# Kernel optimization log

Measured on AMD Instinct MI355X. Metric: run time of the kernel, lower is better.

The kernel has to match this reference:

```python
import math
import jax, jax.numpy as jnp
import numpy as np

LMAX = 2


def _cg_complex(j1, m1, j2, m2, j3, m3):
    # Standard (Racah) Clebsch-Gordan coefficient <j1 m1 j2 m2 | j3 m3> for integer l.
    if m1 + m2 != m3 or j3 < abs(j1 - j2) or j3 > j1 + j2:
        return 0.0
    f = math.factorial
    pre = math.sqrt((2 * j3 + 1) * f(j3 + j1 - j2) * f(j3 - j1 + j2) * f(j1 + j2 - j3) / f(j1 + j2 + j3 + 1))
    pre *= math.sqrt(f(j3 + m3) * f(j3 - m3) * f(j1 - m1) * f(j1 + m1) * f(j2 - m2) * f(j2 + m2))
    kmin = max(0, j2 - j3 - m1, j1 + m2 - j3)
    kmax = min(j1 + j2 - j3, j1 - m1, j2 + m2)
    s = 0.0
    for k in range(kmin, kmax + 1):
        s += (-1.0) ** k / (f(k) * f(j1 + j2 - j3 - k) * f(j1 - m1 - k) * f(j2 + m2 - k) * f(j3 - j2 + m1 + k) * f(j3 - j1 - m2 + k))
    return pre * s


def _u_matrix(l):
    # Unitary map from complex SH (Condon-Shortley) to real SH, rows = real mu, cols = complex m.
    U = np.zeros((2 * l + 1, 2 * l + 1), dtype=np.complex128)
    U[l, l] = 1.0
    isq2 = 1.0 / math.sqrt(2.0)
    for m in range(1, l + 1):
        U[l + m, l - m] = isq2
        U[l + m, l + m] = ((-1.0) ** m) * isq2
        U[l - m, l - m] = 1j * isq2
        U[l - m, l + m] = -1j * ((-1.0) ** m) * isq2
    return U


def _real_clebsch_gordan(lmax):
    # Dense real-SH CG tensor over combined s=(l,m) indices, shape [S,S,S], S=(lmax+1)^2.
    S = (lmax + 1) ** 2
    cg = np.zeros((S, S, S))
    for l1 in range(lmax + 1):
        for l2 in range(lmax + 1):
            for l3 in range(abs(l1 - l2), min(lmax, l1 + l2) + 1):
                blk = np.zeros((2 * l1 + 1, 2 * l2 + 1, 2 * l3 + 1))
                for i1, m1 in enumerate(range(-l1, l1 + 1)):
                    for i2, m2 in enumerate(range(-l2, l2 + 1)):
                        for i3, m3 in enumerate(range(-l3, l3 + 1)):
                            blk[i1, i2, i3] = _cg_complex(l1, m1, l2, m2, l3, m3)
                U1, U2, U3 = _u_matrix(l1), _u_matrix(l2), _u_matrix(l3)
                r = np.einsum('am,bn,co,mno->abc', U1, U2, U3.conj(), blk.astype(np.complex128))
                r = r.real if (l1 + l2 + l3) % 2 == 0 else r.imag  # parity-dependent real part
                cg[l1 * l1:(l1 + 1) ** 2, l2 * l2:(l2 + 1) ** 2, l3 * l3:(l3 + 1) ** 2] = r
    return cg


def _sparse_cg(lmax):
    cg = _real_clebsch_gordan(lmax)
    i1, i2, i3 = np.nonzero(np.abs(cg) > 1e-10)
    vals = cg[i1, i2, i3].astype(np.float32)
    widx = np.floor(np.sqrt(i3.astype(np.float64))).astype(np.int32)  # l of output combined index
    return vals, i1.astype(np.int32), i2.astype(np.int32), i3.astype(np.int32), widx


def _spherical_harmonics_l2(d):
    # Real SH up to l=2, 'component' normalization (|x|=1 assumed). Order: (l,m) = (0,0),(1,-1),(1,0),(1,1),(2,-2..2).
    x, y, z = d[..., 0], d[..., 1], d[..., 2]
    s3, s5, s15 = math.sqrt(3.0), math.sqrt(5.0), math.sqrt(15.0)
    return jnp.stack([
        jnp.ones_like(x),
        s3 * y, s3 * z, s3 * x,
        s15 * x * y, s15 * y * z, 0.5 * s5 * (3.0 * z * z - 1.0), s15 * x * z, 0.5 * s15 * (x * x - y * y),
    ], axis=-1)


def setup_inputs():
    N_ATOMS, N_EDGES, N_BASIS, N_RADIAL = 1200, 12000, 128, 20
    S = (LMAX + 1) ** 2
    key = jax.random.key(0)
    ks = jax.random.split(key, 8)
    vals, i1, i2, i3, widx = _sparse_cg(LMAX)
    return {
        'x': jax.random.normal(ks[0], (N_ATOMS, S, N_BASIS), jnp.float32),
        'radial_ij': jax.random.uniform(ks[1], (N_EDGES, N_RADIAL), jnp.float32),
        'dir_ij': jax.random.normal(ks[2], (N_EDGES, 3), jnp.float32),
        'cutoff_ij': jax.random.uniform(ks[3], (N_EDGES, 1), jnp.float32),
        'W_filter': jax.random.normal(ks[6], (N_RADIAL, N_BASIS * (LMAX + 1)), jnp.float32) / math.sqrt(N_RADIAL),
        'b_filter': jnp.zeros((N_BASIS * (LMAX + 1),), jnp.float32),
        'cg_vals': jnp.asarray(vals),
        'idx_i': jax.random.randint(ks[4], (N_EDGES,), 0, N_ATOMS),
        'idx_j': jax.random.randint(ks[5], (N_EDGES,), 0, N_ATOMS),
        'cg_idx_in1': jnp.asarray(i1),
        'cg_idx_in2': jnp.asarray(i2),
        'cg_idx_out': jnp.asarray(i3),
        'w_idx': jnp.asarray(widx),
    }


def reference(x, radial_ij, dir_ij, cutoff_ij, W_filter, b_filter, cg_vals,
              idx_i, idx_j, cg_idx_in1, cg_idx_in2, cg_idx_out, w_idx):
    n_atoms, S, F = x.shape
    E = dir_ij.shape[0]
    d = dir_ij / jnp.linalg.norm(dir_ij, axis=-1, keepdims=True)
    Y = _spherical_harmonics_l2(d)                        # [E, S]
    Wij = (radial_ij @ W_filter + b_filter) * cutoff_ij   # [E, (lmax+1)*F]
    Wij = Wij.reshape(E, LMAX + 1, F)                     # per-l radial filter
    xj = x[idx_j]                                         # [E, S, F] neighbor features
    # Sparse CG tensor-product contraction over combined (l,m) indices.
    v = (Y[:, cg_idx_in2, None] * cg_vals[None, :, None]
         * Wij[:, w_idx, :] * xj[:, cg_idx_in1, :])       # [E, n_cg, F]
    yij = jnp.zeros((E, S, F), v.dtype).at[:, cg_idx_out, :].add(v)
    return jax.ops.segment_sum(yij, idx_i, num_segments=n_atoms)
```

## Files before the change

### kernel.cpp

```cpp
#include <hip/hip_runtime.h>
#include <math.h>


#define S9     9
#define MROW   12
#define MSZ    (S9 * MROW)
#define NF     128
#define NRAD   20
#define G      4
#define WAVES  4
#define CAP    64

__device__ inline float2 f2fma(float a, float2 b, float2 c) {
    return make_float2(fmaf(a, b.x, c.x), fmaf(a, b.y, c.y));
}

__global__ __launch_bounds__(256) void bucket_kernel(
    const int* __restrict__ idx_i, int E,
    int* __restrict__ cnt,
    int* __restrict__ buck)
{
    int e = blockIdx.x * 256 + threadIdx.x;
    if (e < E) {
        int a = idx_i[e];
        int p = atomicAdd(&cnt[a], 1);
        if (p < CAP) buck[a * CAP + p] = e;
    }
}

__global__ __launch_bounds__(256) void so3_atom_kernel(
    const float* __restrict__ x,
    const float* __restrict__ radial,
    const float* __restrict__ dir,
    const float* __restrict__ cutoff,
    const float* __restrict__ Wf,
    const float* __restrict__ bf,
    const float* __restrict__ cg_vals,
    const int* __restrict__ idx_j,
    const int* __restrict__ cg_i1,
    const int* __restrict__ cg_i2,
    const int* __restrict__ cg_i3,
    int ncg,
    const int* __restrict__ cnt,
    const int* __restrict__ buck,
    float* __restrict__ out)
{
    const int a    = blockIdx.x;
    const int t    = threadIdx.x;
    const int lane = t & 63;
    const int wid  = t >> 6;

    __shared__ __align__(16) float Msh[WAVES][G][MSZ];
    __shared__ float Ysh[WAVES][G][S9];
    __shared__ float radsh[WAVES][G][NRAD];
    __shared__ float cutsh[WAVES][G];
    __shared__ int   egsh[WAVES][G];
    __shared__ float red[WAVES - 1][S9 * NF];

    const int deg = min(cnt[a], CAP);
    const int cw = (deg > wid) ? ((deg - wid + WAVES - 1) / WAVES) : 0;

    float2 acc[S9];
    #pragma unroll
    for (int s = 0; s < S9; ++s) acc[s] = make_float2(0.f, 0.f);

    const float2 b0 = ((const float2*)(bf + 0 * NF))[lane];
    const float2 b1 = ((const float2*)(bf + 1 * NF))[lane];
    const float2 b2 = ((const float2*)(bf + 2 * NF))[lane];

    for (int k0 = 0; k0 < cw; k0 += G) {
        const int ng = min(G, cw - k0);

        if (lane < G) {
            int e = 0; float cut = 0.f;
            if (lane < ng) {
                e = buck[a * CAP + wid + WAVES * (k0 + lane)];
                cut = cutoff[e];
                float dx = dir[3 * e], dy = dir[3 * e + 1], dz = dir[3 * e + 2];
                const float inv = rsqrtf(dx * dx + dy * dy + dz * dz);
                dx *= inv; dy *= inv; dz *= inv;
                const float s3c  = 1.7320508075688772f;
                const float s5c  = 2.2360679774997896f;
                const float s15c = 3.8729833462074170f;
                Ysh[wid][lane][0] = 1.0f;
                Ysh[wid][lane][1] = s3c * dy;
                Ysh[wid][lane][2] = s3c * dz;
                Ysh[wid][lane][3] = s3c * dx;
                Ysh[wid][lane][4] = s15c * dx * dy;
                Ysh[wid][lane][5] = s15c * dy * dz;
                Ysh[wid][lane][6] = 0.5f * s5c * (3.0f * dz * dz - 1.0f);
                Ysh[wid][lane][7] = s15c * dx * dz;
                Ysh[wid][lane][8] = 0.5f * s15c * (dx * dx - dy * dy);
            }
            egsh[wid][lane] = e;
            cutsh[wid][lane] = cut;
        }
        {
            float4* Mz = (float4*)&Msh[wid][0][0];
            #pragma unroll
            for (int qq = lane; qq < G * 27; qq += 64)
                Mz[qq] = make_float4(0.f, 0.f, 0.f, 0.f);
        }
        #pragma unroll
        for (int qq = lane; qq < G * NRAD; qq += 64) {
            const int c = qq / NRAD;
            const int r = qq - c * NRAD;
            float v = 0.f;
            if (c < ng) v = radial[(size_t)egsh[wid][c] * NRAD + r];
            radsh[wid][c][r] = v;
        }

        float2 w[G][3];
        #pragma unroll
        for (int c = 0; c < G; ++c) { w[c][0] = b0; w[c][1] = b1; w[c][2] = b2; }
        #pragma unroll 4
        for (int r = 0; r < NRAD; ++r) {
            const float2* wrow = (const float2*)(Wf + r * (3 * NF));
            const float2 w0 = wrow[lane];
            const float2 w1 = wrow[lane + 64];
            const float2 w2 = wrow[lane + 128];
            #pragma unroll
            for (int c = 0; c < G; ++c) {
                const float rv = radsh[wid][c][r];
                w[c][0] = f2fma(rv, w0, w[c][0]);
                w[c][1] = f2fma(rv, w1, w[c][1]);
                w[c][2] = f2fma(rv, w2, w[c][2]);
            }
        }
        #pragma unroll
        for (int c = 0; c < G; ++c) {
            const float cut = cutsh[wid][c];
            w[c][0].x *= cut; w[c][0].y *= cut;
            w[c][1].x *= cut; w[c][1].y *= cut;
            w[c][2].x *= cut; w[c][2].y *= cut;
        }

        {
            const int c = lane >> 4;
            const int r = lane & 15;
            if (c < ng) {
                for (int k = r; k < ncg; k += 16) {
                    atomicAdd(&Msh[wid][c][cg_i3[k] * MROW + cg_i1[k]],
                              cg_vals[k] * Ysh[wid][c][cg_i2[k]]);
                }
            }
        }

        #pragma unroll
        for (int c = 0; c < G; ++c) {
            if (c < ng) {
                const int e = __builtin_amdgcn_readfirstlane(egsh[wid][c]);
                const int j = __builtin_amdgcn_readfirstlane(idx_j[e]);
                const float2* xp = (const float2*)(x + (size_t)j * (S9 * NF)) + lane;
                float2 xj[S9];
                #pragma unroll
                for (int s = 0; s < S9; ++s) xj[s] = xp[s * 64];

                #pragma unroll
                for (int s3 = 0; s3 < S9; ++s3) {
                    const float4* mr = (const float4*)&Msh[wid][c][s3 * MROW];
                    const float4 m0 = mr[0];
                    const float4 m1 = mr[1];
                    const float  m8 = Msh[wid][c][s3 * MROW + 8];
                    float2 tsum = make_float2(0.f, 0.f);
                    tsum = f2fma(m0.x, xj[0], tsum);
                    tsum = f2fma(m0.y, xj[1], tsum);
                    tsum = f2fma(m0.z, xj[2], tsum);
                    tsum = f2fma(m0.w, xj[3], tsum);
                    tsum = f2fma(m1.x, xj[4], tsum);
                    tsum = f2fma(m1.y, xj[5], tsum);
                    tsum = f2fma(m1.z, xj[6], tsum);
                    tsum = f2fma(m1.w, xj[7], tsum);
                    tsum = f2fma(m8,   xj[8], tsum);
                    const float2 wl = (s3 == 0) ? w[c][0] : ((s3 < 4) ? w[c][1] : w[c][2]);
                    acc[s3].x = fmaf(wl.x, tsum.x, acc[s3].x);
                    acc[s3].y = fmaf(wl.y, tsum.y, acc[s3].y);
                }
            }
        }
    }

    if (wid > 0) {
        float2* rp = (float2*)&red[wid - 1][0];
        #pragma unroll
        for (int s = 0; s < S9; ++s) rp[s * 64 + lane] = acc[s];
    }
    __syncthreads();
    if (wid == 0) {
        #pragma unroll
        for (int r2 = 0; r2 < WAVES - 1; ++r2) {
            const float2* rp = (const float2*)&red[r2][0];
            #pragma unroll
            for (int s = 0; s < S9; ++s) {
                float2 v = rp[s * 64 + lane];
                acc[s].x += v.x; acc[s].y += v.y;
            }
        }
        float2* op = (float2*)(out + (size_t)a * (S9 * NF)) + lane;
        #pragma unroll
        for (int s = 0; s < S9; ++s) op[s * 64] = acc[s];
    }
}

__global__ __launch_bounds__(256) void so3_edge_fused(
    const float* __restrict__ x, const float* __restrict__ radial,
    const float* __restrict__ dir, const float* __restrict__ cutoff,
    const float* __restrict__ Wf, const float* __restrict__ bf,
    const float* __restrict__ cg_vals,
    const int* __restrict__ idx_i, const int* __restrict__ idx_j,
    const int* __restrict__ cg_i1, const int* __restrict__ cg_i2,
    const int* __restrict__ cg_i3, int ncg, int E,
    float* __restrict__ out)
{
    const int wid  = threadIdx.x >> 6;
    const int lane = threadIdx.x & 63;
    const int e = blockIdx.x * 4 + wid;
    if (e >= E) return;

    __shared__ __align__(16) float Msh[4][MSZ];
    __shared__ float Ysh[4][S9];

    if (lane < 27) ((float4*)&Msh[wid][0])[lane] = make_float4(0.f, 0.f, 0.f, 0.f);

    float dx = dir[3 * e], dy = dir[3 * e + 1], dz = dir[3 * e + 2];
    const float inv = rsqrtf(dx * dx + dy * dy + dz * dz);
    dx *= inv; dy *= inv; dz *= inv;
    if (lane == 0) {
        const float s3c = 1.7320508075688772f, s5c = 2.2360679774997896f,
                    s15c = 3.8729833462074170f;
        Ysh[wid][0] = 1.0f;
        Ysh[wid][1] = s3c * dy; Ysh[wid][2] = s3c * dz; Ysh[wid][3] = s3c * dx;
        Ysh[wid][4] = s15c * dx * dy; Ysh[wid][5] = s15c * dy * dz;
        Ysh[wid][6] = 0.5f * s5c * (3.0f * dz * dz - 1.0f);
        Ysh[wid][7] = s15c * dx * dz;
        Ysh[wid][8] = 0.5f * s15c * (dx * dx - dy * dy);
    }
    for (int k = lane; k < ncg; k += 64)
        atomicAdd(&Msh[wid][cg_i3[k] * MROW + cg_i1[k]], cg_vals[k] * Ysh[wid][cg_i2[k]]);

    float rad[NRAD];
    #pragma unroll
    for (int r = 0; r < NRAD; ++r) rad[r] = radial[(size_t)e * NRAD + r];
    const float cut = cutoff[e];

    float2 w0 = ((const float2*)(bf + 0 * NF))[lane];
    float2 w1 = ((const float2*)(bf + 1 * NF))[lane];
    float2 w2 = ((const float2*)(bf + 2 * NF))[lane];
    #pragma unroll 4
    for (int r = 0; r < NRAD; ++r) {
        const float2* wrow = (const float2*)(Wf + r * (3 * NF));
        w0 = f2fma(rad[r], wrow[lane], w0);
        w1 = f2fma(rad[r], wrow[lane + 64], w1);
        w2 = f2fma(rad[r], wrow[lane + 128], w2);
    }
    w0.x *= cut; w0.y *= cut; w1.x *= cut; w1.y *= cut; w2.x *= cut; w2.y *= cut;

    const int j = __builtin_amdgcn_readfirstlane(idx_j[e]);
    const float2* xp = (const float2*)(x + (size_t)j * (S9 * NF)) + lane;
    float2 xj[S9];
    #pragma unroll
    for (int s = 0; s < S9; ++s) xj[s] = xp[s * 64];

    const int a = __builtin_amdgcn_readfirstlane(idx_i[e]);
    float* op = out + (size_t)a * (S9 * NF) + 2 * lane;
    #pragma unroll
    for (int s3 = 0; s3 < S9; ++s3) {
        const float4* mr = (const float4*)&Msh[wid][s3 * MROW];
        const float4 m0 = mr[0];
        const float4 m1 = mr[1];
        const float  m8 = Msh[wid][s3 * MROW + 8];
        float2 tsum = make_float2(0.f, 0.f);
        tsum = f2fma(m0.x, xj[0], tsum);
        tsum = f2fma(m0.y, xj[1], tsum);
        tsum = f2fma(m0.z, xj[2], tsum);
        tsum = f2fma(m0.w, xj[3], tsum);
        tsum = f2fma(m1.x, xj[4], tsum);
        tsum = f2fma(m1.y, xj[5], tsum);
        tsum = f2fma(m1.z, xj[6], tsum);
        tsum = f2fma(m1.w, xj[7], tsum);
        tsum = f2fma(m8,   xj[8], tsum);
        const float2 wl = (s3 == 0) ? w0 : ((s3 < 4) ? w1 : w2);
        atomicAdd(&op[s3 * NF],     wl.x * tsum.x);
        atomicAdd(&op[s3 * NF + 1], wl.y * tsum.y);
    }
}

extern "C" void kernel_launch(void* const* d_in, const int* in_sizes, int n_in,
                              void* d_out, int out_size, void* d_ws, size_t ws_size,
                              hipStream_t stream) {
    const float* x       = (const float*)d_in[0];
    const float* radial  = (const float*)d_in[1];
    const float* dir     = (const float*)d_in[2];
    const float* cutoff  = (const float*)d_in[3];
    const float* Wf      = (const float*)d_in[4];
    const float* bf      = (const float*)d_in[5];
    const float* cg_vals = (const float*)d_in[6];
    const int*   idx_i   = (const int*)d_in[7];
    const int*   idx_j   = (const int*)d_in[8];
    const int*   cg_i1   = (const int*)d_in[9];
    const int*   cg_i2   = (const int*)d_in[10];
    const int*   cg_i3   = (const int*)d_in[11];

    const int E   = in_sizes[7];
    const int ncg = in_sizes[6];
    const int A   = in_sizes[0] / (S9 * NF);

    size_t need = ((size_t)(A + 1) + (size_t)A * CAP) * sizeof(int);

    if (ws_size >= need) {
        int* cnt  = (int*)d_ws;
        int* buck = cnt + (A + 1);

        hipMemsetAsync(cnt, 0, (size_t)(A + 1) * sizeof(int), stream);

        bucket_kernel<<<(E + 255) / 256, 256, 0, stream>>>(idx_i, E, cnt, buck);

        so3_atom_kernel<<<A, 256, 0, stream>>>(
            x, radial, dir, cutoff, Wf, bf, cg_vals, idx_j,
            cg_i1, cg_i2, cg_i3, ncg, cnt, buck, (float*)d_out);
    } else {
        hipMemsetAsync(d_out, 0, (size_t)out_size * sizeof(float), stream);
        so3_edge_fused<<<(E + 3) / 4, 256, 0, stream>>>(
            x, radial, dir, cutoff, Wf, bf, cg_vals, idx_i, idx_j,
            cg_i1, cg_i2, cg_i3, ncg, E, (float*)d_out);
    }
}
```

Measured before the change: 152.5 us.

## Split atom work into edge chunks with CG cell presort and separate reduction

Replaces the per-atom 4-wave block with single-wave blocks that each handle a chunk of 8 edges, writing partial sums to workspace slots that a new reduce kernel combines. The CG contraction is presorted into (s3,s1) cells in a prep kernel, so building the per-edge coupling matrix needs no shared-memory atomics. The intent is more parallel blocks, better load balance and cheaper M construction. The cost is an extra kernel launch, the slot traffic through global memory, and idle lanes when chunks are only partly filled.

```diff
diff --git a/kernel.cpp b/kernel.cpp
--- a/kernel.cpp
+++ b/kernel.cpp
@@ -7,74 +7,111 @@
 #define MSZ    (S9 * MROW)
 #define NF     128
 #define NRAD   20
-#define G      4
-#define WAVES  4
+#define CEDGE  8
+#define NCHUNK 3
 #define CAP    64
+#define NCELL  81
+#define MAXCG  512
 
 __device__ inline float2 f2fma(float a, float2 b, float2 c) {
     return make_float2(fmaf(a, b.x, c.x), fmaf(a, b.y, c.y));
 }
 
-__global__ __launch_bounds__(256) void bucket_kernel(
-    const int* __restrict__ idx_i, int E,
+__global__ __launch_bounds__(256) void prep_kernel(
+    const int* __restrict__ idx_i, int E, int nbuck,
+    const int* __restrict__ cg_i1, const int* __restrict__ cg_i2,
+    const int* __restrict__ cg_i3, const float* __restrict__ cg_vals, int ncg,
     int* __restrict__ cnt,
-    int* __restrict__ buck)
+    int* __restrict__ buck,
+    int* __restrict__ cellOff,
+    int2* __restrict__ cellDat)
 {
-    int e = blockIdx.x * 256 + threadIdx.x;
-    if (e < E) {
-        int a = idx_i[e];
-        int p = atomicAdd(&cnt[a], 1);
-        if (p < CAP) buck[a * CAP + p] = e;
-    }
-}
-
-__global__ __launch_bounds__(256) void so3_atom_kernel(
+    const int t = threadIdx.x;
+    if ((int)blockIdx.x < nbuck) {
+        int e = blockIdx.x * 256 + t;
+        if (e < E) {
+            int a = idx_i[e];
+            int p = atomicAdd(&cnt[a], 1);
+            if (p < CAP) buck[a * CAP + p] = e;
+        }
+        return;
+    }
+    __shared__ int hist[NCELL];
+    __shared__ int cur[NCELL];
+    if (t < NCELL) hist[t] = 0;
+    __syncthreads();
+    for (int k = t; k < ncg; k += 256)
+        atomicAdd(&hist[cg_i3[k] * S9 + cg_i1[k]], 1);
+    __syncthreads();
+    if (t == 0) {
+        int run = 0;
+        for (int c = 0; c < NCELL; ++c) {
+            cellOff[c] = run; cur[c] = run; run += hist[c];
+        }
+        cellOff[NCELL] = run;
+    }
+    __syncthreads();
+    for (int k = t; k < ncg; k += 256) {
+        int cell = cg_i3[k] * S9 + cg_i1[k];
+        int p = atomicAdd(&cur[cell], 1);
+        cellDat[p] = make_int2(cg_i2[k], __float_as_int(cg_vals[k]));
+    }
+}
+
+__global__ __launch_bounds__(64) void so3_chunk_kernel(
     const float* __restrict__ x,
     const float* __restrict__ radial,
     const float* __restrict__ dir,
     const float* __restrict__ cutoff,
     const float* __restrict__ Wf,
     const float* __restrict__ bf,
-    const float* __restrict__ cg_vals,
     const int* __restrict__ idx_j,
-    const int* __restrict__ cg_i1,
-    const int* __restrict__ cg_i2,
-    const int* __restrict__ cg_i3,
-    int ncg,
     const int* __restrict__ cnt,
     const int* __restrict__ buck,
-    float* __restrict__ out)
+    const int* __restrict__ cellOff,
+    const int2* __restrict__ cellDat,
+    int ncg,
+    float* __restrict__ slots)
 {
-    const int a    = blockIdx.x;
-    const int t    = threadIdx.x;
-    const int lane = t & 63;
-    const int wid  = t >> 6;
-
-    __shared__ __align__(16) float Msh[WAVES][G][MSZ];
-    __shared__ float Ysh[WAVES][G][S9];
-    __shared__ float radsh[WAVES][G][NRAD];
-    __shared__ float cutsh[WAVES][G];
-    __shared__ int   egsh[WAVES][G];
-    __shared__ float red[WAVES - 1][S9 * NF];
+    const int a = blockIdx.x / NCHUNK;
+    const int q = blockIdx.x - a * NCHUNK;
+    const int t = threadIdx.x;
 
     const int deg = min(cnt[a], CAP);
-    const int cw = (deg > wid) ? ((deg - wid + WAVES - 1) / WAVES) : 0;
+    if (q > 0 && q * CEDGE >= deg) return;
+
+    __shared__ __align__(16) float M[CEDGE][MSZ];
+    __shared__ float Ysh[CEDGE][S9];
+    __shared__ float radsh[CEDGE][NRAD];
+    __shared__ float cutsh[CEDGE];
+    __shared__ int   egsh[CEDGE];
+    __shared__ int   jsh[CEDGE];
+    __shared__ int   offsh[NCELL + 1];
+    __shared__ int2  datsh[MAXCG];
+
+    for (int k = t; k <= NCELL; k += 64) offsh[k] = cellOff[k];
+    for (int k = t; k < ncg; k += 64) datsh[k] = cellDat[k];
 
     float2 acc[S9];
     #pragma unroll
     for (int s = 0; s < S9; ++s) acc[s] = make_float2(0.f, 0.f);
 
-    const float2 b0 = ((const float2*)(bf + 0 * NF))[lane];
-    const float2 b1 = ((const float2*)(bf + 1 * NF))[lane];
-    const float2 b2 = ((const float2*)(bf + 2 * NF))[lane];
-
-    for (int k0 = 0; k0 < cw; k0 += G) {
-        const int ng = min(G, cw - k0);
-
-        if (lane < G) {
-            int e = 0; float cut = 0.f;
-            if (lane < ng) {
-                e = buck[a * CAP + wid + WAVES * (k0 + lane)];
+    const float2 b0 = ((const float2*)(bf + 0 * NF))[t];
+    const float2 b1 = ((const float2*)(bf + 1 * NF))[t];
+    const float2 b2 = ((const float2*)(bf + 2 * NF))[t];
+
+    int base = q * CEDGE;
+    do {
+        const int n = min(CEDGE, deg - base);
+
+        if (t < CEDGE) {
+            int e = 0, jj = a;
+            float cut = 0.f;
+            float y0 = 0.f, y1 = 0.f, y2 = 0.f, y3 = 0.f, y4 = 0.f,
+                  y5 = 0.f, y6 = 0.f, y7 = 0.f, y8 = 0.f;
+            if (t < n) {
+                e = buck[a * CAP + base + t];
+                jj = idx_j[e];
                 cut = cutoff[e];
                 float dx = dir[3 * e], dy = dir[3 * e + 1], dz = dir[3 * e + 2];
                 const float inv = rsqrtf(dx * dx + dy * dy + dz * dz);
@@ -82,124 +119,134 @@
                 const float s3c  = 1.7320508075688772f;
                 const float s5c  = 2.2360679774997896f;
                 const float s15c = 3.8729833462074170f;
-                Ysh[wid][lane][0] = 1.0f;
-                Ysh[wid][lane][1] = s3c * dy;
-                Ysh[wid][lane][2] = s3c * dz;
-                Ysh[wid][lane][3] = s3c * dx;
-                Ysh[wid][lane][4] = s15c * dx * dy;
-                Ysh[wid][lane][5] = s15c * dy * dz;
-                Ysh[wid][lane][6] = 0.5f * s5c * (3.0f * dz * dz - 1.0f);
-                Ysh[wid][lane][7] = s15c * dx * dz;
-                Ysh[wid][lane][8] = 0.5f * s15c * (dx * dx - dy * dy);
+                y0 = 1.0f;
+                y1 = s3c * dy; y2 = s3c * dz; y3 = s3c * dx;
+                y4 = s15c * dx * dy; y5 = s15c * dy * dz;
+                y6 = 0.5f * s5c * (3.0f * dz * dz - 1.0f);
+                y7 = s15c * dx * dz;
+                y8 = 0.5f * s15c * (dx * dx - dy * dy);
             }
-            egsh[wid][lane] = e;
-            cutsh[wid][lane] = cut;
-        }
-        {
-            float4* Mz = (float4*)&Msh[wid][0][0];
-            #pragma unroll
-            for (int qq = lane; qq < G * 27; qq += 64)
-                Mz[qq] = make_float4(0.f, 0.f, 0.f, 0.f);
-        }
-        #pragma unroll
-        for (int qq = lane; qq < G * NRAD; qq += 64) {
+            egsh[t] = e; jsh[t] = jj; cutsh[t] = cut;
+            Ysh[t][0] = y0; Ysh[t][1] = y1; Ysh[t][2] = y2;
+            Ysh[t][3] = y3; Ysh[t][4] = y4; Ysh[t][5] = y5;
+            Ysh[t][6] = y6; Ysh[t][7] = y7; Ysh[t][8] = y8;
+        }
+        for (int qq = t; qq < CEDGE * NRAD; qq += 64) {
             const int c = qq / NRAD;
             const int r = qq - c * NRAD;
             float v = 0.f;
-            if (c < ng) v = radial[(size_t)egsh[wid][c] * NRAD + r];
-            radsh[wid][c][r] = v;
-        }
-
-        float2 w[G][3];
-        #pragma unroll
-        for (int c = 0; c < G; ++c) { w[c][0] = b0; w[c][1] = b1; w[c][2] = b2; }
+            if (c < n) v = radial[(size_t)egsh[c] * NRAD + r];
+            radsh[c][r] = v;
+        }
+
+        float2 w[CEDGE][3];
+        #pragma unroll
+        for (int c = 0; c < CEDGE; ++c) { w[c][0] = b0; w[c][1] = b1; w[c][2] = b2; }
         #pragma unroll 4
         for (int r = 0; r < NRAD; ++r) {
             const float2* wrow = (const float2*)(Wf + r * (3 * NF));
-            const float2 w0 = wrow[lane];
-            const float2 w1 = wrow[lane + 64];
-            const float2 w2 = wrow[lane + 128];
+            const float2 w0 = wrow[t];
+            const float2 w1 = wrow[t + 64];
+            const float2 w2 = wrow[t + 128];
             #pragma unroll
-            for (int c = 0; c < G; ++c) {
-                const float rv = radsh[wid][c][r];
+            for (int c = 0; c < CEDGE; ++c) {
+                const float rv = radsh[c][r];
                 w[c][0] = f2fma(rv, w0, w[c][0]);
                 w[c][1] = f2fma(rv, w1, w[c][1]);
                 w[c][2] = f2fma(rv, w2, w[c][2]);
             }
         }
         #pragma unroll
-        for (int c = 0; c < G; ++c) {
-            const float cut = cutsh[wid][c];
+        for (int c = 0; c < CEDGE; ++c) {
+            const float cut = cutsh[c];
             w[c][0].x *= cut; w[c][0].y *= cut;
             w[c][1].x *= cut; w[c][1].y *= cut;
             w[c][2].x *= cut; w[c][2].y *= cut;
         }
 
-        {
-            const int c = lane >> 4;
-            const int r = lane & 15;
-            if (c < ng) {
-                for (int k = r; k < ncg; k += 16) {
-                    atomicAdd(&Msh[wid][c][cg_i3[k] * MROW + cg_i1[k]],
-                              cg_vals[k] * Ysh[wid][c][cg_i2[k]]);
+        #pragma unroll
+        for (int cc = 0; cc < 2; ++cc) {
+            const int cell = t + cc * 64;
+            if (cell < NCELL) {
+                const int s3i = cell / 9;
+                const int s1i = cell - 9 * s3i;
+                const int o0 = offsh[cell], o1 = offsh[cell + 1];
+                float m[CEDGE];
+                #pragma unroll
+                for (int c = 0; c < CEDGE; ++c) m[c] = 0.f;
+                for (int idx = o0; idx < o1; ++idx) {
+                    const int2 d = datsh[idx];
+                    const float v = __int_as_float(d.y);
+                    #pragma unroll
+                    for (int c = 0; c < CEDGE; ++c)
+                        m[c] = fmaf(v, Ysh[c][d.x], m[c]);
                 }
+                #pragma unroll
+                for (int c = 0; c < CEDGE; ++c) M[c][s3i * MROW + s1i] = m[c];
             }
         }
 
         #pragma unroll
-        for (int c = 0; c < G; ++c) {
-            if (c < ng) {
-                const int e = __builtin_amdgcn_readfirstlane(egsh[wid][c]);
-                const int j = __builtin_amdgcn_readfirstlane(idx_j[e]);
-                const float2* xp = (const float2*)(x + (size_t)j * (S9 * NF)) + lane;
-                float2 xj[S9];
-                #pragma unroll
-                for (int s = 0; s < S9; ++s) xj[s] = xp[s * 64];
-
-                #pragma unroll
-                for (int s3 = 0; s3 < S9; ++s3) {
-                    const float4* mr = (const float4*)&Msh[wid][c][s3 * MROW];
-                    const float4 m0 = mr[0];
-                    const float4 m1 = mr[1];
-                    const float  m8 = Msh[wid][c][s3 * MROW + 8];
-                    float2 tsum = make_float2(0.f, 0.f);
-                    tsum = f2fma(m0.x, xj[0], tsum);
-                    tsum = f2fma(m0.y, xj[1], tsum);
-                    tsum = f2fma(m0.z, xj[2], tsum);
-                    tsum = f2fma(m0.w, xj[3], tsum);
-                    tsum = f2fma(m1.x, xj[4], tsum);
-                    tsum = f2fma(m1.y, xj[5], tsum);
-                    tsum = f2fma(m1.z, xj[6], tsum);
-                    tsum = f2fma(m1.w, xj[7], tsum);
-                    tsum = f2fma(m8,   xj[8], tsum);
-                    const float2 wl = (s3 == 0) ? w[c][0] : ((s3 < 4) ? w[c][1] : w[c][2]);
-                    acc[s3].x = fmaf(wl.x, tsum.x, acc[s3].x);
-                    acc[s3].y = fmaf(wl.y, tsum.y, acc[s3].y);
-                }
+        for (int c = 0; c < CEDGE; ++c) {
+            const int j = __builtin_amdgcn_readfirstlane(jsh[c]);
+            const float2* xp = (const float2*)(x + (size_t)j * (S9 * NF)) + t;
+            float2 xj[S9];
+            #pragma unroll
+            for (int s = 0; s < S9; ++s) xj[s] = xp[s * 64];
+
+            #pragma unroll
+            for (int s3 = 0; s3 < S9; ++s3) {
+                const float4* mr = (const float4*)&M[c][s3 * MROW];
+                const float4 m0 = mr[0];
+                const float4 m1 = mr[1];
+                const float  m8 = M[c][s3 * MROW + 8];
+                float2 tsum = make_float2(0.f, 0.f);
+                tsum = f2fma(m0.x, xj[0], tsum);
+                tsum = f2fma(m0.y, xj[1], tsum);
+                tsum = f2fma(m0.z, xj[2], tsum);
+                tsum = f2fma(m0.w, xj[3], tsum);
+                tsum = f2fma(m1.x, xj[4], tsum);
+                tsum = f2fma(m1.y, xj[5], tsum);
+                tsum = f2fma(m1.z, xj[6], tsum);
+                tsum = f2fma(m1.w, xj[7], tsum);
+                tsum = f2fma(m8,   xj[8], tsum);
+                const float2 wl = (s3 == 0) ? w[c][0] : ((s3 < 4) ? w[c][1] : w[c][2]);
+                acc[s3].x = fmaf(wl.x, tsum.x, acc[s3].x);
+                acc[s3].y = fmaf(wl.y, tsum.y, acc[s3].y);
             }
         }
-    }
-
-    if (wid > 0) {
-        float2* rp = (float2*)&red[wid - 1][0];
-        #pragma unroll
-        for (int s = 0; s < S9; ++s) rp[s * 64 + lane] = acc[s];
-    }
-    __syncthreads();
-    if (wid == 0) {
-        #pragma unroll
-        for (int r2 = 0; r2 < WAVES - 1; ++r2) {
-            const float2* rp = (const float2*)&red[r2][0];
-            #pragma unroll
-            for (int s = 0; s < S9; ++s) {
-                float2 v = rp[s * 64 + lane];
-                acc[s].x += v.x; acc[s].y += v.y;
-            }
-        }
-        float2* op = (float2*)(out + (size_t)a * (S9 * NF)) + lane;
-        #pragma unroll
-        for (int s = 0; s < S9; ++s) op[s * 64] = acc[s];
-    }
+        base += CEDGE;
+    } while (q == NCHUNK - 1 && base < deg);
+
+    float2* sp = (float2*)(slots + (size_t)(a * NCHUNK + q) * (S9 * NF)) + t;
+    #pragma unroll
+    for (int s = 0; s < S9; ++s) sp[s * 64] = acc[s];
+}
+
+__global__ __launch_bounds__(64) void reduce_kernel(
+    const float* __restrict__ slots, const int* __restrict__ cnt,
+    float* __restrict__ out)
+{
+    const int a = blockIdx.x;
+    const int t = threadIdx.x;
+    const int deg = min(cnt[a], CAP);
+    const int nch = min((deg + CEDGE - 1) / CEDGE, NCHUNK);
+
+    float2 acc[S9];
+    #pragma unroll
+    for (int s = 0; s < S9; ++s) acc[s] = make_float2(0.f, 0.f);
+
+    for (int q = 0; q < nch; ++q) {
+        const float2* sp = (const float2*)(slots + (size_t)(a * NCHUNK + q) * (S9 * NF)) + t;
+        #pragma unroll
+        for (int s = 0; s < S9; ++s) {
+            float2 v = sp[s * 64];
+            acc[s].x += v.x; acc[s].y += v.y;
+        }
+    }
+    float2* op = (float2*)(out + (size_t)a * (S9 * NF)) + t;
+    #pragma unroll
+    for (int s = 0; s < S9; ++s) op[s * 64] = acc[s];
 }
 
 __global__ __launch_bounds__(256) void so3_edge_fused(
@@ -305,19 +352,29 @@
     const int ncg = in_sizes[6];
     const int A   = in_sizes[0] / (S9 * NF);
 
-    size_t need = ((size_t)(A + 1) + (size_t)A * CAP) * sizeof(int);
-
-    if (ws_size >= need) {
-        int* cnt  = (int*)d_ws;
-        int* buck = cnt + (A + 1);
-
-        hipMemsetAsync(cnt, 0, (size_t)(A + 1) * sizeof(int), stream);
-
-        bucket_kernel<<<(E + 255) / 256, 256, 0, stream>>>(idx_i, E, cnt, buck);
-
-        so3_atom_kernel<<<A, 256, 0, stream>>>(
-            x, radial, dir, cutoff, Wf, bf, cg_vals, idx_j,
-            cg_i1, cg_i2, cg_i3, ncg, cnt, buck, (float*)d_out);
+    int* cnt      = (int*)d_ws;
+    int* cellOff  = cnt + A;
+    int* buck     = cellOff + (NCELL + 1);
+    size_t ib     = (size_t)(A + NCELL + 1 + A * CAP) * sizeof(int);
+    size_t doff   = (ib + 255) & ~(size_t)255;
+    int2* cellDat = (int2*)((char*)d_ws + doff);
+    size_t soff   = (doff + (size_t)ncg * sizeof(int2) + 255) & ~(size_t)255;
+    float* slots  = (float*)((char*)d_ws + soff);
+    size_t need   = soff + (size_t)A * NCHUNK * (S9 * NF) * sizeof(float);
+
+    if (ws_size >= need && ncg <= MAXCG) {
+        hipMemsetAsync(cnt, 0, (size_t)A * sizeof(int), stream);
+
+        const int nbuck = (E + 255) / 256;
+        prep_kernel<<<nbuck + 1, 256, 0, stream>>>(
+            idx_i, E, nbuck, cg_i1, cg_i2, cg_i3, cg_vals, ncg,
+            cnt, buck, cellOff, cellDat);
+
+        so3_chunk_kernel<<<A * NCHUNK, 64, 0, stream>>>(
+            x, radial, dir, cutoff, Wf, bf, idx_j,
+            cnt, buck, cellOff, cellDat, ncg, slots);
+
+        reduce_kernel<<<A, 64, 0, stream>>>(slots, cnt, (float*)d_out);
     } else {
         hipMemsetAsync(d_out, 0, (size_t)out_size * sizeof(float), stream);
         so3_edge_fused<<<(E + 3) / 4, 256, 0, stream>>>(
```

Measured after the change: 123.4 us. 19.1% less time.
